# Performance work log

Hardware: AMD Instinct MI355X
Metric: run time of the kernel (lower is better)

Reference implementation:

```python
import jax, jax.numpy as jnp
import numpy as np

B, T, N = 512, 1024, 64


def setup_inputs() -> dict:
    key = jax.random.key(0)
    k1, k2, k3, k4 = jax.random.split(key, 4)
    inputs = jax.random.normal(k1, (B, T, N), dtype=jnp.float32)
    trans = jax.random.normal(k2, (N, N), dtype=jnp.float32) * 0.1
    tag_indices = jax.random.randint(k3, (B, T), 0, N)
    sequence_lengths = jax.random.randint(k4, (B,), 1, T + 1)  # at least 1
    return {
        "inputs": inputs,
        "trans": trans,
        "tag_indices": tag_indices,
        "sequence_lengths": sequence_lengths,
    }


def _crf_log_likelihood(inputs, trans, tag_indices, sequence_lengths):
    Bn, Tn, Nn = inputs.shape
    # mask[b, t] = 1 if t < length[b]
    mask = (jnp.arange(Tn)[None, :] < sequence_lengths[:, None]).astype(inputs.dtype)

    # unary score: sum_t inputs[b, t, tag[b, t]] * mask
    unary = jnp.take_along_axis(inputs, tag_indices[..., None], axis=2)[..., 0]  # [B, T]
    unary_score = jnp.sum(unary * mask, axis=1)

    # binary score: sum_t trans[tag[t], tag[t+1]] masked by mask[:, 1:]
    binary = trans[tag_indices[:, :-1], tag_indices[:, 1:]]  # [B, T-1]
    binary_score = jnp.sum(binary * mask[:, 1:], axis=1)

    sequence_scores = unary_score + binary_score

    # log normalizer via forward algorithm (logsumexp recurrence)
    first = inputs[:, 0]                       # [B, N] initial alphas
    rest = jnp.swapaxes(inputs[:, 1:], 0, 1)   # [T-1, B, N] time-major
    steps = jnp.arange(Tn - 1)

    def step(alpha, xt):
        x, t = xt  # x: [B, N]
        # alpha[b, i] + trans[i, j], logsumexp over i
        new = x + jax.nn.logsumexp(alpha[:, :, None] + trans[None, :, :], axis=1)
        # dynamic_rnn with sequence_length = len - 1: stop updating past the end
        upd = (t < sequence_lengths - 1)[:, None]
        return jnp.where(upd, new, alpha), None

    alpha, _ = jax.lax.scan(step, first, (rest, steps))
    log_norm = jax.nn.logsumexp(alpha, axis=1)  # [B]

    return sequence_scores - log_norm


def reference(inputs, trans, tag_indices, sequence_lengths):
    return _crf_log_likelihood(inputs, trans, tag_indices, sequence_lengths)
```

## Files before the change

kernel.cpp:

```cpp
#include <hip/hip_runtime.h>
#include <math.h>

#define Bn 512
#define Tn 1024
#define Nn 64
#define LOG2E_F 1.44269504088896340736f
#define LN2_F   0.69314718055994530942f

__device__ __forceinline__ float wave_max(float v) {
    #pragma unroll
    for (int o = 32; o > 0; o >>= 1) v = fmaxf(v, __shfl_xor(v, o));
    return v;
}
__device__ __forceinline__ float wave_sum(float v) {
    #pragma unroll
    for (int o = 32; o > 0; o >>= 1) v += __shfl_xor(v, o);
    return v;
}

__global__ __launch_bounds__(256) void crf_scores(
    const float* __restrict__ inputs, const float* __restrict__ trans,
    const int* __restrict__ tags, const int* __restrict__ lens,
    float* __restrict__ out)
{
    const int b = blockIdx.x;
    const int L = lens[b];
    const int* tagb = tags + b * Tn;
    const float* inb = inputs + (size_t)b * Tn * Nn;

    float acc = 0.f;
    for (int t = threadIdx.x; t < L; t += 256) {
        int tg = tagb[t];
        acc += inb[t * Nn + tg];
        if (t >= 1) acc += trans[tagb[t - 1] * Nn + tg];
    }
    acc = wave_sum(acc);
    __shared__ float red[4];
    if ((threadIdx.x & 63) == 0) red[threadIdx.x >> 6] = acc;
    __syncthreads();
    if (threadIdx.x == 0) out[b] = (red[0] + red[1]) + (red[2] + red[3]);
}


#define DOT_LDS(dst) do {                                          \
    float _s0 = 0.f, _s1 = 0.f, _s2 = 0.f, _s3 = 0.f;             \
    _Pragma("unroll")                                              \
    for (int _i = 0; _i < 64; _i += 4) {                           \
        float4 _qv = *(const float4*)&shq[_i];                     \
        _s0 = fmaf(_qv.x, E[_i    ], _s0);                         \
        _s1 = fmaf(_qv.y, E[_i + 1], _s1);                         \
        _s2 = fmaf(_qv.z, E[_i + 2], _s2);                         \
        _s3 = fmaf(_qv.w, E[_i + 3], _s3);                         \
    }                                                              \
    (dst) = (_s0 + _s1) + (_s2 + _s3);                             \
} while (0)

#define STEPX(BWDV, EXV) do {                                      \
    shq[j] = (BWDV) ? ((EXV) * q) : q;                             \
    float _s; DOT_LDS(_s);                                         \
    q = (BWDV) ? _s : ((EXV) * _s);                                \
} while (0)

#define RENORM() do {                                              \
    float _m = wave_max(q);                                        \
    q *= (1.0f / _m);                                              \
    base += __logf(_m);                                            \
} while (0)

__device__ __forceinline__ int clamp_row(int tt, int Lm1) {
    return tt < 0 ? 0 : (tt > Lm1 ? Lm1 : tt);
}

template <bool FULL>
__global__ __launch_bounds__(64, 1) void crf_fwdbwd(
    const float* __restrict__ inputs, const float* __restrict__ trans,
    const int* __restrict__ lens, float* __restrict__ ws,
    float* __restrict__ out)
{
    const int j = threadIdx.x;
    const bool bwd = (!FULL) && (blockIdx.x >= Bn);
    const int b = bwd ? (blockIdx.x - Bn) : blockIdx.x;
    const int L = lens[b];
    const int Lm1 = L - 1;
    const float* inb = inputs + (size_t)b * Tn * Nn;

    float E[64];
    __shared__ float trsh[64 * 65];
    __shared__ __align__(16) float shq[64];
    if (!bwd) {
        #pragma unroll
        for (int i = 0; i < 64; ++i) E[i] = exp2f(trans[i * 64 + j] * LOG2E_F);
    } else {
        #pragma unroll
        for (int i = 0; i < 64; ++i) trsh[i * 65 + j] = trans[i * 64 + j];
        __syncthreads();
        #pragma unroll
        for (int i = 0; i < 64; ++i) E[i] = exp2f(trsh[j * 65 + i] * LOG2E_F);
    }

    float q, base;
    int t0, dir, n;
    const int tf = L >> 1;
    if (!bwd) {
        float x0 = inb[j];
        float m = wave_max(x0);
        q = exp2f((x0 - m) * LOG2E_F);
        base = m;
        t0 = 1; dir = 1;
        n = FULL ? (L - 1) : tf;
    } else {
        q = 1.f; base = 0.f;
        t0 = L - 1; dir = -1;
        n = (L - 1) - tf;
    }

    float xc[8];
    #pragma unroll
    for (int d = 0; d < 8; ++d)
        xc[d] = inb[clamp_row(t0 + d * dir, Lm1) * Nn + j];

    int t = t0;
    int k = 0;
    if (!bwd) {
        while (k + 8 <= n) {
            float xn[8];
            #pragma unroll
            for (int d = 0; d < 8; ++d)
                xn[d] = inb[clamp_row(t + (8 + d) * dir, Lm1) * Nn + j];
            #pragma unroll
            for (int u = 0; u < 8; ++u) {
                float exu = exp2f(fmaf(xc[u], LOG2E_F, -6.0f));
                STEPX(false, exu);
            }
            RENORM();
            #pragma unroll
            for (int d = 0; d < 8; ++d) xc[d] = xn[d];
            k += 8; t += 8;
        }
        #pragma unroll
        for (int u = 0; u < 8; ++u) {
            if (k + u < n) {
                float exu = exp2f(fmaf(xc[u], LOG2E_F, -6.0f));
                STEPX(false, exu);
            }
        }
    } else {
        while (k + 8 <= n) {
            float xn[8];
            #pragma unroll
            for (int d = 0; d < 8; ++d)
                xn[d] = inb[clamp_row(t - (8 + d), Lm1) * Nn + j];
            #pragma unroll
            for (int u = 0; u < 8; ++u) {
                float exu = exp2f(fmaf(xc[u], LOG2E_F, -6.0f));
                STEPX(true, exu);
            }
            RENORM();
            #pragma unroll
            for (int d = 0; d < 8; ++d) xc[d] = xn[d];
            k += 8; t -= 8;
        }
        #pragma unroll
        for (int u = 0; u < 8; ++u) {
            if (k + u < n) {
                float exu = exp2f(fmaf(xc[u], LOG2E_F, -6.0f));
                STEPX(true, exu);
            }
        }
    }

    {
        float m = wave_max(q);
        q *= (1.0f / m);
        base += __logf(m) + LN2_F * 6.0f * (float)n;
    }

    if (FULL) {
        float ssum = wave_sum(q);
        if (j == 0) out[b] -= (base + __logf(ssum));
    } else {
        float* fvec = ws;
        float* gvec = ws + Bn * 64;
        float* fb   = ws + 2 * Bn * 64;
        float* gb   = fb + Bn;
        if (!bwd) { fvec[b * 64 + j] = q; if (j == 0) fb[b] = base; }
        else      { gvec[b * 64 + j] = q; if (j == 0) gb[b] = base; }
    }
}

__global__ __launch_bounds__(64, 1) void crf_combine(
    const float* __restrict__ ws, float* __restrict__ out)
{
    const int b = blockIdx.x;
    const int j = threadIdx.x;
    const float* fvec = ws;
    const float* gvec = ws + Bn * 64;
    const float* fb   = ws + 2 * Bn * 64;
    const float* gb   = fb + Bn;

    float p = wave_sum(fvec[b * 64 + j] * gvec[b * 64 + j]);
    if (j == 0) out[b] -= (__logf(p) + fb[b] + gb[b]);
}

extern "C" void kernel_launch(void* const* d_in, const int* in_sizes, int n_in,
                              void* d_out, int out_size, void* d_ws, size_t ws_size,
                              hipStream_t stream) {
    const float* inputs = (const float*)d_in[0];
    const float* trans  = (const float*)d_in[1];
    const int*   tags   = (const int*)d_in[2];
    const int*   lens   = (const int*)d_in[3];
    float* out = (float*)d_out;
    float* ws  = (float*)d_ws;

    crf_scores<<<Bn, 256, 0, stream>>>(inputs, trans, tags, lens, out);

    const size_t need = (size_t)(2 * Bn * 64 + 2 * Bn) * sizeof(float);
    if (ws_size >= need) {
        crf_fwdbwd<false><<<2 * Bn, 64, 0, stream>>>(inputs, trans, lens, ws, out);
        crf_combine<<<Bn, 64, 0, stream>>>(ws, out);
    } else {
        crf_fwdbwd<true><<<Bn, 64, 0, stream>>>(inputs, trans, lens, ws, out);
    }
}
```

Measured before the change: 355.4 us.

## Split matvec across half-waves with cross-lane shuffle and defer renormalization

```diff
diff --git a/kernel.cpp b/kernel.cpp
--- a/kernel.cpp
+++ b/kernel.cpp
@@ -42,29 +42,38 @@
 }
 
 
-#define DOT_LDS(dst) do {                                          \
-    float _s0 = 0.f, _s1 = 0.f, _s2 = 0.f, _s3 = 0.f;             \
+#define STEP2(BWDV, EXV) do {                                      \
+    shq[j] = (BWDV) ? ((EXV) * q) : q;                             \
+    float4 _qv[8];                                                 \
     _Pragma("unroll")                                              \
-    for (int _i = 0; _i < 64; _i += 4) {                           \
-        float4 _qv = *(const float4*)&shq[_i];                     \
-        _s0 = fmaf(_qv.x, E[_i    ], _s0);                         \
-        _s1 = fmaf(_qv.y, E[_i + 1], _s1);                         \
-        _s2 = fmaf(_qv.z, E[_i + 2], _s2);                         \
-        _s3 = fmaf(_qv.w, E[_i + 3], _s3);                         \
+    for (int _cb = 0; _cb < 8; ++_cb)                              \
+        _qv[_cb] = *(const float4*)&shq[(g << 5) + (_cb << 2)];    \
+    float _aP0 = 0.f, _aP1 = 0.f, _aQ0 = 0.f, _aQ1 = 0.f;         \
+    _Pragma("unroll")                                              \
+    for (int _cb = 0; _cb < 8; _cb += 2) {                         \
+        const float4 _u0 = _qv[_cb], _u1 = _qv[_cb + 1];           \
+        _aP0 = fmaf(_u0.x, Ef[4*_cb + 0], _aP0);                   \
+        _aQ0 = fmaf(_u0.x, Ef[32 + 4*_cb + 0], _aQ0);              \
+        _aP0 = fmaf(_u0.y, Ef[4*_cb + 1], _aP0);                   \
+        _aQ0 = fmaf(_u0.y, Ef[32 + 4*_cb + 1], _aQ0);              \
+        _aP0 = fmaf(_u0.z, Ef[4*_cb + 2], _aP0);                   \
+        _aQ0 = fmaf(_u0.z, Ef[32 + 4*_cb + 2], _aQ0);              \
+        _aP0 = fmaf(_u0.w, Ef[4*_cb + 3], _aP0);                   \
+        _aQ0 = fmaf(_u0.w, Ef[32 + 4*_cb + 3], _aQ0);              \
+        _aP1 = fmaf(_u1.x, Ef[4*_cb + 4], _aP1);                   \
+        _aQ1 = fmaf(_u1.x, Ef[32 + 4*_cb + 4], _aQ1);              \
+        _aP1 = fmaf(_u1.y, Ef[4*_cb + 5], _aP1);                   \
+        _aQ1 = fmaf(_u1.y, Ef[32 + 4*_cb + 5], _aQ1);              \
+        _aP1 = fmaf(_u1.z, Ef[4*_cb + 6], _aP1);                   \
+        _aQ1 = fmaf(_u1.z, Ef[32 + 4*_cb + 6], _aQ1);              \
+        _aP1 = fmaf(_u1.w, Ef[4*_cb + 7], _aP1);                   \
+        _aQ1 = fmaf(_u1.w, Ef[32 + 4*_cb + 7], _aQ1);              \
     }                                                              \
-    (dst) = (_s0 + _s1) + (_s2 + _s3);                             \
-} while (0)
-
-#define STEPX(BWDV, EXV) do {                                      \
-    shq[j] = (BWDV) ? ((EXV) * q) : q;                             \
-    float _s; DOT_LDS(_s);                                         \
+    float _aP = _aP0 + _aP1, _aQ = _aQ0 + _aQ1;                    \
+    float _u = lo32 ? _aP : _aQ;                                   \
+    float _w = lo32 ? _aQ : _aP;                                   \
+    float _s = _u + __shfl_xor(_w, 32);                            \
     q = (BWDV) ? _s : ((EXV) * _s);                                \
-} while (0)
-
-#define RENORM() do {                                              \
-    float _m = wave_max(q);                                        \
-    q *= (1.0f / _m);                                              \
-    base += __logf(_m);                                            \
 } while (0)
 
 __device__ __forceinline__ int clamp_row(int tt, int Lm1) {
@@ -78,24 +87,33 @@
     float* __restrict__ out)
 {
     const int j = threadIdx.x;
+    const int g = j >> 5;
+    const int p = j & 31;
+    const bool lo32 = (j < 32);
     const bool bwd = (!FULL) && (blockIdx.x >= Bn);
     const int b = bwd ? (blockIdx.x - Bn) : blockIdx.x;
     const int L = lens[b];
     const int Lm1 = L - 1;
     const float* inb = inputs + (size_t)b * Tn * Nn;
 
-    float E[64];
+    float Ef[64];
     __shared__ float trsh[64 * 65];
     __shared__ __align__(16) float shq[64];
     if (!bwd) {
         #pragma unroll
-        for (int i = 0; i < 64; ++i) E[i] = exp2f(trans[i * 64 + j] * LOG2E_F);
+        for (int c = 0; c < 32; ++c) {
+            Ef[c]      = exp2f(trans[(g * 32 + c) * 64 + p     ] * LOG2E_F);
+            Ef[32 + c] = exp2f(trans[(g * 32 + c) * 64 + p + 32] * LOG2E_F);
+        }
     } else {
         #pragma unroll
         for (int i = 0; i < 64; ++i) trsh[i * 65 + j] = trans[i * 64 + j];
         __syncthreads();
         #pragma unroll
-        for (int i = 0; i < 64; ++i) E[i] = exp2f(trsh[j * 65 + i] * LOG2E_F);
+        for (int c = 0; c < 32; ++c) {
+            Ef[c]      = exp2f(trsh[p        * 65 + g * 32 + c] * LOG2E_F);
+            Ef[32 + c] = exp2f(trsh[(p + 32) * 65 + g * 32 + c] * LOG2E_F);
+        }
     }
 
     float q, base;
@@ -121,27 +139,34 @@
 
     int t = t0;
     int k = 0;
+    float pend = 1.0f;
+
     if (!bwd) {
         while (k + 8 <= n) {
             float xn[8];
             #pragma unroll
             for (int d = 0; d < 8; ++d)
                 xn[d] = inb[clamp_row(t + (8 + d) * dir, Lm1) * Nn + j];
-            #pragma unroll
-            for (int u = 0; u < 8; ++u) {
-                float exu = exp2f(fmaf(xc[u], LOG2E_F, -6.0f));
-                STEPX(false, exu);
-            }
-            RENORM();
+            float exc[8];
+            #pragma unroll
+            for (int u = 0; u < 8; ++u)
+                exc[u] = exp2f(fmaf(xc[u], LOG2E_F, -6.0f));
+            exc[2] *= pend;
+            #pragma unroll
+            for (int u = 0; u < 8; ++u) STEP2(false, exc[u]);
+            float m = wave_max(q);
+            base += __logf(m);
+            pend = 1.0f / m;
             #pragma unroll
             for (int d = 0; d < 8; ++d) xc[d] = xn[d];
             k += 8; t += 8;
         }
+        q *= pend; pend = 1.0f;
         #pragma unroll
         for (int u = 0; u < 8; ++u) {
             if (k + u < n) {
                 float exu = exp2f(fmaf(xc[u], LOG2E_F, -6.0f));
-                STEPX(false, exu);
+                STEP2(false, exu);
             }
         }
     } else {
@@ -150,21 +175,26 @@
             #pragma unroll
             for (int d = 0; d < 8; ++d)
                 xn[d] = inb[clamp_row(t - (8 + d), Lm1) * Nn + j];
-            #pragma unroll
-            for (int u = 0; u < 8; ++u) {
-                float exu = exp2f(fmaf(xc[u], LOG2E_F, -6.0f));
-                STEPX(true, exu);
-            }
-            RENORM();
+            float exc[8];
+            #pragma unroll
+            for (int u = 0; u < 8; ++u)
+                exc[u] = exp2f(fmaf(xc[u], LOG2E_F, -6.0f));
+            exc[2] *= pend;
+            #pragma unroll
+            for (int u = 0; u < 8; ++u) STEP2(true, exc[u]);
+            float m = wave_max(q);
+            base += __logf(m);
+            pend = 1.0f / m;
             #pragma unroll
             for (int d = 0; d < 8; ++d) xc[d] = xn[d];
             k += 8; t -= 8;
         }
+        q *= pend; pend = 1.0f;
         #pragma unroll
         for (int u = 0; u < 8; ++u) {
             if (k + u < n) {
                 float exu = exp2f(fmaf(xc[u], LOG2E_F, -6.0f));
-                STEPX(true, exu);
+                STEP2(true, exu);
             }
         }
     }
```

Result: faster. 313.1 us (-11.9%).
